# Kernel optimization log

Hardware: AMD Instinct MI355X
Metric: run time of the kernel (lower is better)

## Reference

```python
import jax, jax.numpy as jnp
import numpy as np

N_NODES = 100000
HIDDEN = 64
IN_CH = 61


def setup_inputs() -> dict:
    key = jax.random.key(0)
    ks = jax.random.split(key, 12)
    x = jax.random.normal(ks[0], (N_NODES, IN_CH), dtype=jnp.float32)
    edge_index = jax.random.randint(ks[1], (2, 3200000), 0, N_NODES, dtype=jnp.int64)
    s = 0.1
    # GCNConv weights (lin: in->hidden, bias separate)
    W1 = jax.random.normal(ks[2], (IN_CH, HIDDEN), dtype=jnp.float32) * s
    b1 = jnp.zeros((HIDDEN,), dtype=jnp.float32)
    W2 = jax.random.normal(ks[3], (HIDDEN, HIDDEN), dtype=jnp.float32) * s
    b2 = jnp.zeros((HIDDEN,), dtype=jnp.float32)
    W3 = jax.random.normal(ks[4], (HIDDEN, HIDDEN), dtype=jnp.float32) * s
    b3 = jnp.zeros((HIDDEN,), dtype=jnp.float32)
    # MLP head: Linear(64,64) -> ReLU -> Linear(64,1)
    Wh1 = jax.random.normal(ks[5], (HIDDEN, HIDDEN), dtype=jnp.float32) * s
    bh1 = jnp.zeros((HIDDEN,), dtype=jnp.float32)
    Wh2 = jax.random.normal(ks[6], (HIDDEN, 1), dtype=jnp.float32) * s
    bh2 = jnp.zeros((1,), dtype=jnp.float32)
    return {"x": x, "edge_index": edge_index,
            "W1": W1, "b1": b1, "W2": W2, "b2": b2, "W3": W3, "b3": b3,
            "Wh1": Wh1, "bh1": bh1, "Wh2": Wh2, "bh2": bh2}


def _gcn_layer(x, W, b, src, dst, norm, n):
    # x' = scatter_add_{dst}( norm_e * (xW)[src] ) + b   (self-loops already in src/dst)
    h = x @ W                                    # (N, out)
    msg = norm[:, None] * h[src]                 # (E', out) gather
    agg = jax.ops.segment_sum(msg, dst, num_segments=n)  # scatter-add
    return agg + b


def reference(x, edge_index, W1, b1, W2, b2, W3, b3, Wh1, bh1, Wh2, bh2):
    n = x.shape[0]
    # add self-loops (GCNConv default add_self_loops=True)
    loop = jnp.arange(n, dtype=edge_index.dtype)
    src = jnp.concatenate([edge_index[0], loop])
    dst = jnp.concatenate([edge_index[1], loop])
    # symmetric normalization: deg from in-degree (dst), norm = d^-1/2[src]*d^-1/2[dst]
    deg = jax.ops.segment_sum(jnp.ones_like(dst, dtype=x.dtype), dst, num_segments=n)
    dinv = jnp.where(deg > 0, jax.lax.rsqrt(deg), 0.0)
    norm = dinv[src] * dinv[dst]
    h = x
    for (W, b) in ((W1, b1), (W2, b2), (W3, b3)):
        h = jax.nn.relu(_gcn_layer(h, W, b, src, dst, norm, n))
        # dropout: identity in eval mode
    # MLP head
    h = jax.nn.relu(h @ Wh1 + bh1)
    out = (h @ Wh2 + bh2).squeeze(-1)            # (N,)
    return out
```

## Files before the change

### kernel.cpp

```cpp
#include <hip/hip_runtime.h>
#include <hip/hip_fp16.h>

#define HID 64
#define FSH 8
#define FB 392
#define SCAP 9216
#define FCH 4096

__device__ __forceinline__ float2 h2f2(unsigned int bits) {
    __half2 h = __builtin_bit_cast(__half2, bits);
    return __half22float2(h);
}

__global__ void zero_kernel(int* __restrict__ p, int n) {
    int i = blockIdx.x * blockDim.x + threadIdx.x;
    if (i < n) p[i] = 0;
}

__global__ __launch_bounds__(256) void fillA_kernel(const int* __restrict__ src,
                                                    const int* __restrict__ dst,
                                                    int* __restrict__ gcur,
                                                    unsigned int* __restrict__ recA,
                                                    int E) {
    __shared__ unsigned int srec[FCH];
    __shared__ int hist[FB], lbase[FB], lcur[FB], gpos[FB];
    __shared__ int buf[256];
    int t = threadIdx.x;
    int base = blockIdx.x * FCH;
    int lim = E - base;
    if (lim > FCH) lim = FCH;
    if (lim <= 0) return;
    for (int i = t; i < FB; i += 256) hist[i] = 0;
    __syncthreads();
    for (int i = t; i < lim; i += 256) atomicAdd(&hist[dst[base + i] >> FSH], 1);
    __syncthreads();
    int i0 = 2 * t, i1 = 2 * t + 1;
    int a0 = (i0 < FB) ? hist[i0] : 0;
    int a1 = (i1 < FB) ? hist[i1] : 0;
    int pair = a0 + a1;
    buf[t] = pair;
    __syncthreads();
#pragma unroll
    for (int o = 1; o < 256; o <<= 1) {
        int v = (t >= o) ? buf[t - o] : 0;
        __syncthreads();
        buf[t] += v;
        __syncthreads();
    }
    int excl = buf[t] - pair;
    if (i0 < FB) { lbase[i0] = excl;      lcur[i0] = excl; }
    if (i1 < FB) { lbase[i1] = excl + a0; lcur[i1] = excl + a0; }
    __syncthreads();
    for (int i = t; i < FB; i += 256) gpos[i] = atomicAdd(&gcur[i], hist[i]);
    __syncthreads();
    for (int i = t; i < lim; i += 256) {
        int d = dst[base + i];
        int s = src[base + i];
        int bkt = d >> FSH;
        int idx = atomicAdd(&lcur[bkt], 1);
        srec[idx] = ((unsigned int)(d & ((1 << FSH) - 1)) << 17) | (unsigned int)s;
    }
    __syncthreads();
    int g16 = t >> 4, lane = t & 15;
    for (int bkt = g16; bkt < FB; bkt += 16) {
        int L = hist[bkt], lb = lbase[bkt], gp = gpos[bkt];
        for (int j = lane; j < L; j += 16) {
            int g = gp + j;
            if (g < SCAP) recA[(size_t)bkt * SCAP + g] = srec[lb + j];
        }
    }
}

__global__ __launch_bounds__(256) void fillB_kernel(const int* __restrict__ gcur,
                                                    const unsigned int* __restrict__ recA,
                                                    int* __restrict__ rowptr,
                                                    float* __restrict__ dinv,
                                                    int* __restrict__ col, int N) {
    __shared__ unsigned int lcol[SCAP];
    __shared__ int hist[256], cur[256], buf[256];
    int b = blockIdx.x, t = threadIdx.x;
    int n0 = b << FSH;
    int p = 0;
    for (int i = t; i < b; i += 256) p += min(gcur[i], SCAP);
    buf[t] = p;
    __syncthreads();
#pragma unroll
    for (int o = 128; o > 0; o >>= 1) {
        if (t < o) buf[t] += buf[t + o];
        __syncthreads();
    }
    int rbase = buf[0];
    __syncthreads();
    hist[t] = 0;
    __syncthreads();
    int cnt = gcur[b];
    if (cnt > SCAP) cnt = SCAP;
    const unsigned int* rA = recA + (size_t)b * SCAP;
    for (int r = t; r < cnt; r += 256) atomicAdd(&hist[rA[r] >> 17], 1);
    __syncthreads();
    int a = hist[t];
    buf[t] = a;
    __syncthreads();
#pragma unroll
    for (int o = 1; o < 256; o <<= 1) {
        int v = (t >= o) ? buf[t - o] : 0;
        __syncthreads();
        buf[t] += v;
        __syncthreads();
    }
    int excl = buf[t] - a;
    int node = n0 + t;
    if (node <= N) rowptr[node] = rbase + excl;
    if (node < N) dinv[node] = 1.0f / sqrtf((float)(a + 1));
    cur[t] = excl;
    __syncthreads();
    for (int r = t; r < cnt; r += 256) {
        unsigned int rec = rA[r];
        int pos = atomicAdd(&cur[rec >> 17], 1);
        lcol[pos] = rec & 0x1ffffu;
    }
    __syncthreads();
    for (int j = t; j < cnt; j += 256) col[rbase + j] = (int)lcol[j];
}

__global__ __launch_bounds__(256) void linscale61_kernel(const float* __restrict__ x,
                                                         const float* __restrict__ W,
                                                         const float* __restrict__ dinv,
                                                         __half* __restrict__ out, int N) {
    __shared__ float4 Wl[61 * 16];
    const float4* W4 = reinterpret_cast<const float4*>(W);
    for (int i = threadIdx.x; i < 61 * 16; i += blockDim.x) Wl[i] = W4[i];
    __syncthreads();
    int node = blockIdx.x * blockDim.x + threadIdx.x;
    if (node >= N) return;
    float4 acc[16];
#pragma unroll
    for (int c = 0; c < 16; ++c) acc[c] = make_float4(0.f, 0.f, 0.f, 0.f);
    const float* xr = x + (size_t)node * 61;
    for (int k = 0; k < 61; ++k) {
        float xv = xr[k];
#pragma unroll
        for (int c = 0; c < 16; ++c) {
            float4 w = Wl[k * 16 + c];
            acc[c].x += xv * w.x;
            acc[c].y += xv * w.y;
            acc[c].z += xv * w.z;
            acc[c].w += xv * w.w;
        }
    }
    float dv = dinv[node];
    __half2* o = reinterpret_cast<__half2*>(out + (size_t)node * HID);
#pragma unroll
    for (int c = 0; c < 16; ++c) {
        o[c * 2 + 0] = __floats2half2_rn(acc[c].x * dv, acc[c].y * dv);
        o[c * 2 + 1] = __floats2half2_rn(acc[c].z * dv, acc[c].w * dv);
    }
}

__global__ __launch_bounds__(256) void linscale64h_kernel(const __half* __restrict__ x,
                                                          const float* __restrict__ W,
                                                          const float* __restrict__ dinv,
                                                          __half* __restrict__ out, int N) {
    __shared__ float4 Wl[64 * 16];
    const float4* W4 = reinterpret_cast<const float4*>(W);
    for (int i = threadIdx.x; i < 64 * 16; i += blockDim.x) Wl[i] = W4[i];
    __syncthreads();
    int node = blockIdx.x * blockDim.x + threadIdx.x;
    if (node >= N) return;
    float4 acc[16];
#pragma unroll
    for (int c = 0; c < 16; ++c) acc[c] = make_float4(0.f, 0.f, 0.f, 0.f);
    const uint4* xr4 = reinterpret_cast<const uint4*>(x + ((size_t)node << 6));
#pragma unroll
    for (int c8 = 0; c8 < 8; ++c8) {
        uint4 pk = xr4[c8];
        float2 f0 = h2f2(pk.x), f1 = h2f2(pk.y), f2 = h2f2(pk.z), f3 = h2f2(pk.w);
        float xv[8] = {f0.x, f0.y, f1.x, f1.y, f2.x, f2.y, f3.x, f3.y};
#pragma unroll
        for (int j = 0; j < 8; ++j) {
            int k = c8 * 8 + j;
#pragma unroll
            for (int c = 0; c < 16; ++c) {
                float4 w = Wl[k * 16 + c];
                acc[c].x += xv[j] * w.x;
                acc[c].y += xv[j] * w.y;
                acc[c].z += xv[j] * w.z;
                acc[c].w += xv[j] * w.w;
            }
        }
    }
    float dv = dinv[node];
    __half2* o = reinterpret_cast<__half2*>(out + ((size_t)node << 6));
#pragma unroll
    for (int c = 0; c < 16; ++c) {
        o[c * 2 + 0] = __floats2half2_rn(acc[c].x * dv, acc[c].y * dv);
        o[c * 2 + 1] = __floats2half2_rn(acc[c].z * dv, acc[c].w * dv);
    }
}

__global__ __launch_bounds__(256) void gather_kernel(const int* __restrict__ rowptr,
                                                     const int* __restrict__ col,
                                                     const float* __restrict__ dinv,
                                                     const __half2* __restrict__ hs2,
                                                     const float* __restrict__ b,
                                                     __half2* __restrict__ out2, int N) {
    int lane = threadIdx.x & 63;
    int hf = lane >> 5;
    int gl = lane & 31;
    int wid = (blockIdx.x * blockDim.x + threadIdx.x) >> 6;
    int nw = (gridDim.x * blockDim.x) >> 6;
    float bx = b[2 * gl], by = b[2 * gl + 1];
    for (int dbase = wid * 2; dbase < N; dbase += nw * 2) {
        int d = dbase + hf;
        bool act = d < N;
        int dd = act ? d : N - 1;
        int beg = rowptr[dd];
        int end = act ? rowptr[dd + 1] : beg;
        float2 acc0 = __half22float2(hs2[((size_t)dd << 5) + gl]);
        float2 acc1 = make_float2(0.f, 0.f);
        for (int ebase = beg; ebase < end; ebase += 32) {
            int e = ebase + gl;
            int cv = (e < end) ? col[e] : 0;
            int cnt = end - ebase;
            {
                unsigned int r[16];
#pragma unroll
                for (int k = 0; k < 16; ++k) {
                    int s = __shfl(cv, k, 32);
                    r[k] = *reinterpret_cast<const unsigned int*>(hs2 + ((size_t)s << 5) + gl);
                }
#pragma unroll
                for (int k = 0; k < 16; ++k) {
                    unsigned int bits = (k < cnt) ? r[k] : 0u;
                    float2 v = h2f2(bits);
                    if (k & 1) { acc1.x += v.x; acc1.y += v.y; }
                    else       { acc0.x += v.x; acc0.y += v.y; }
                }
            }
            if (cnt > 16) {
                unsigned int r[16];
#pragma unroll
                for (int k = 0; k < 16; ++k) {
                    int s = __shfl(cv, k + 16, 32);
                    r[k] = *reinterpret_cast<const unsigned int*>(hs2 + ((size_t)s << 5) + gl);
                }
#pragma unroll
                for (int k = 0; k < 16; ++k) {
                    unsigned int bits = (k + 16 < cnt) ? r[k] : 0u;
                    float2 v = h2f2(bits);
                    if (k & 1) { acc1.x += v.x; acc1.y += v.y; }
                    else       { acc0.x += v.x; acc0.y += v.y; }
                }
            }
        }
        if (act) {
            float dv = dinv[d];
            float rx = fmaxf(fmaf(acc0.x + acc1.x, dv, bx), 0.f);
            float ry = fmaxf(fmaf(acc0.y + acc1.y, dv, by), 0.f);
            out2[((size_t)d << 5) + gl] = __floats2half2_rn(rx, ry);
        }
    }
}

__global__ __launch_bounds__(256) void head_kernel(const __half* __restrict__ h,
                                                   const float* __restrict__ Wh1,
                                                   const float* __restrict__ bh1,
                                                   const float* __restrict__ Wh2,
                                                   const float* __restrict__ bh2,
                                                   float* __restrict__ out, int N) {
    __shared__ float4 Wl[64 * 16];
    __shared__ float bhs[64];
    __shared__ float w2s[64];
    const float4* W4 = reinterpret_cast<const float4*>(Wh1);
    for (int i = threadIdx.x; i < 64 * 16; i += blockDim.x) Wl[i] = W4[i];
    if (threadIdx.x < 64) {
        bhs[threadIdx.x] = bh1[threadIdx.x];
        w2s[threadIdx.x] = Wh2[threadIdx.x];
    }
    __syncthreads();
    int node = blockIdx.x * blockDim.x + threadIdx.x;
    if (node >= N) return;
    float4 acc[16];
#pragma unroll
    for (int c = 0; c < 16; ++c) acc[c] = make_float4(0.f, 0.f, 0.f, 0.f);
    const uint4* hr4 = reinterpret_cast<const uint4*>(h + ((size_t)node << 6));
#pragma unroll
    for (int c8 = 0; c8 < 8; ++c8) {
        uint4 pk = hr4[c8];
        float2 f0 = h2f2(pk.x), f1 = h2f2(pk.y), f2 = h2f2(pk.z), f3 = h2f2(pk.w);
        float xv[8] = {f0.x, f0.y, f1.x, f1.y, f2.x, f2.y, f3.x, f3.y};
#pragma unroll
        for (int j = 0; j < 8; ++j) {
            int k = c8 * 8 + j;
#pragma unroll
            for (int c = 0; c < 16; ++c) {
                float4 w = Wl[k * 16 + c];
                acc[c].x += xv[j] * w.x;
                acc[c].y += xv[j] * w.y;
                acc[c].z += xv[j] * w.z;
                acc[c].w += xv[j] * w.w;
            }
        }
    }
    float o = 0.f;
#pragma unroll
    for (int c = 0; c < 16; ++c) {
        o += fmaxf(acc[c].x + bhs[4 * c + 0], 0.f) * w2s[4 * c + 0];
        o += fmaxf(acc[c].y + bhs[4 * c + 1], 0.f) * w2s[4 * c + 1];
        o += fmaxf(acc[c].z + bhs[4 * c + 2], 0.f) * w2s[4 * c + 2];
        o += fmaxf(acc[c].w + bhs[4 * c + 3], 0.f) * w2s[4 * c + 3];
    }
    out[node] = o + bh2[0];
}

extern "C" void kernel_launch(void* const* d_in, const int* in_sizes, int n_in,
                              void* d_out, int out_size, void* d_ws, size_t ws_size,
                              hipStream_t stream) {
    const float* x = (const float*)d_in[0];
    const int* edge = (const int*)d_in[1];
    const float* W1 = (const float*)d_in[2];
    const float* b1 = (const float*)d_in[3];
    const float* W2 = (const float*)d_in[4];
    const float* b2 = (const float*)d_in[5];
    const float* W3 = (const float*)d_in[6];
    const float* b3 = (const float*)d_in[7];
    const float* Wh1 = (const float*)d_in[8];
    const float* bh1 = (const float*)d_in[9];
    const float* Wh2 = (const float*)d_in[10];
    const float* bh2 = (const float*)d_in[11];

    int N = in_sizes[0] / 61;
    int E = in_sizes[1] / 2;
    const int* srcs = edge;
    const int* dsts = edge + E;
    float* out = (float*)d_out;

    char* ws = (char*)d_ws;
    size_t off = 0;
    auto alloc = [&](size_t bytes) {
        void* p = ws + off;
        off += (bytes + 255) & ~(size_t)255;
        return p;
    };
    float* dinv = (float*)alloc((size_t)N * 4);
    int* rowptr = (int*)alloc((size_t)(N + 1) * 4);
    int* gcur = (int*)alloc((size_t)FB * 4);
    int* col = (int*)alloc((size_t)E * 4);
    __half* Ah = (__half*)alloc((size_t)N * HID * 2);
    __half* Bh = (__half*)alloc((size_t)N * HID * 2);
    if (off > ws_size) return;
    unsigned int* recA = (unsigned int*)Ah;

    int gN = (N + 255) / 256;
    int gA = (E + FCH - 1) / FCH;

    zero_kernel<<<(FB + 255) / 256, 256, 0, stream>>>(gcur, FB);
    fillA_kernel<<<gA, 256, 0, stream>>>(srcs, dsts, gcur, recA, E);
    fillB_kernel<<<FB, 256, 0, stream>>>(gcur, recA, rowptr, dinv, col, N);

    linscale61_kernel<<<gN, 256, 0, stream>>>(x, W1, dinv, Bh, N);
    gather_kernel<<<4096, 256, 0, stream>>>(rowptr, col, dinv,
                                            (const __half2*)Bh, b1, (__half2*)Ah, N);

    linscale64h_kernel<<<gN, 256, 0, stream>>>(Ah, W2, dinv, Bh, N);
    gather_kernel<<<4096, 256, 0, stream>>>(rowptr, col, dinv,
                                            (const __half2*)Bh, b2, (__half2*)Ah, N);

    linscale64h_kernel<<<gN, 256, 0, stream>>>(Ah, W3, dinv, Bh, N);
    gather_kernel<<<4096, 256, 0, stream>>>(rowptr, col, dinv,
                                            (const __half2*)Bh, b3, (__half2*)Ah, N);

    head_kernel<<<gN, 256, 0, stream>>>(Ah, Wh1, bh1, Wh2, bh2, out, N);
}
```

Before: 351.7 us.

## Halve CSR-build bucket width and stage x rows through LDS in first linear

The CSR construction now uses buckets of 128 destination nodes instead of 256. That doubles the bucket count to 784 and halves the per-bucket capacity, so the prefix scan in fillA and the node-level logic in fillB are adapted to the new sizes. fillB gets twice as many blocks with less shared memory each, which should improve occupancy and parallelism. Separately, the first linear kernel now copies each block's 128 rows of x into shared memory with coalesced loads, replacing strided per-thread row reads, and runs with 128-thread blocks. The smaller SCAP raises the chance that a bucket with high in-degree exceeds capacity and has edges silently dropped.

```diff
diff --git a/kernel.cpp b/kernel.cpp
--- a/kernel.cpp
+++ b/kernel.cpp
@@ -2,9 +2,9 @@
 #include <hip/hip_fp16.h>
 
 #define HID 64
-#define FSH 8
-#define FB 392
-#define SCAP 9216
+#define FSH 7
+#define FB 784
+#define SCAP 4608
 #define FCH 4096
 
 __device__ __forceinline__ float2 h2f2(unsigned int bits) {
@@ -34,11 +34,14 @@
     __syncthreads();
     for (int i = t; i < lim; i += 256) atomicAdd(&hist[dst[base + i] >> FSH], 1);
     __syncthreads();
-    int i0 = 2 * t, i1 = 2 * t + 1;
-    int a0 = (i0 < FB) ? hist[i0] : 0;
-    int a1 = (i1 < FB) ? hist[i1] : 0;
-    int pair = a0 + a1;
-    buf[t] = pair;
+    int h[4];
+#pragma unroll
+    for (int j = 0; j < 4; ++j) {
+        int idx = 4 * t + j;
+        h[j] = (idx < FB) ? hist[idx] : 0;
+    }
+    int tsum = h[0] + h[1] + h[2] + h[3];
+    buf[t] = tsum;
     __syncthreads();
 #pragma unroll
     for (int o = 1; o < 256; o <<= 1) {
@@ -47,9 +50,13 @@
         buf[t] += v;
         __syncthreads();
     }
-    int excl = buf[t] - pair;
-    if (i0 < FB) { lbase[i0] = excl;      lcur[i0] = excl; }
-    if (i1 < FB) { lbase[i1] = excl + a0; lcur[i1] = excl + a0; }
+    int excl = buf[t] - tsum;
+#pragma unroll
+    for (int j = 0; j < 4; ++j) {
+        int idx = 4 * t + j;
+        if (idx < FB) { lbase[idx] = excl; lcur[idx] = excl; }
+        excl += h[j];
+    }
     __syncthreads();
     for (int i = t; i < FB; i += 256) gpos[i] = atomicAdd(&gcur[i], hist[i]);
     __syncthreads();
@@ -61,10 +68,10 @@
         srec[idx] = ((unsigned int)(d & ((1 << FSH) - 1)) << 17) | (unsigned int)s;
     }
     __syncthreads();
-    int g16 = t >> 4, lane = t & 15;
-    for (int bkt = g16; bkt < FB; bkt += 16) {
+    int g8 = t >> 3, lane = t & 7;
+    for (int bkt = g8; bkt < FB; bkt += 32) {
         int L = hist[bkt], lb = lbase[bkt], gp = gpos[bkt];
-        for (int j = lane; j < L; j += 16) {
+        for (int j = lane; j < L; j += 8) {
             int g = gp + j;
             if (g < SCAP) recA[(size_t)bkt * SCAP + g] = srec[lb + j];
         }
@@ -77,7 +84,7 @@
                                                     float* __restrict__ dinv,
                                                     int* __restrict__ col, int N) {
     __shared__ unsigned int lcol[SCAP];
-    __shared__ int hist[256], cur[256], buf[256];
+    __shared__ int hist[128], cur[128], buf[256];
     int b = blockIdx.x, t = threadIdx.x;
     int n0 = b << FSH;
     int p = 0;
@@ -91,14 +98,14 @@
     }
     int rbase = buf[0];
     __syncthreads();
-    hist[t] = 0;
+    if (t < 128) hist[t] = 0;
     __syncthreads();
     int cnt = gcur[b];
     if (cnt > SCAP) cnt = SCAP;
     const unsigned int* rA = recA + (size_t)b * SCAP;
     for (int r = t; r < cnt; r += 256) atomicAdd(&hist[rA[r] >> 17], 1);
     __syncthreads();
-    int a = hist[t];
+    int a = (t < 128) ? hist[t] : 0;
     buf[t] = a;
     __syncthreads();
 #pragma unroll
@@ -109,10 +116,12 @@
         __syncthreads();
     }
     int excl = buf[t] - a;
-    int node = n0 + t;
-    if (node <= N) rowptr[node] = rbase + excl;
-    if (node < N) dinv[node] = 1.0f / sqrtf((float)(a + 1));
-    cur[t] = excl;
+    if (t < 128) {
+        int node = n0 + t;
+        if (node <= N) rowptr[node] = rbase + excl;
+        if (node < N) dinv[node] = 1.0f / sqrtf((float)(a + 1));
+        cur[t] = excl;
+    }
     __syncthreads();
     for (int r = t; r < cnt; r += 256) {
         unsigned int rec = rA[r];
@@ -123,20 +132,29 @@
     for (int j = t; j < cnt; j += 256) col[rbase + j] = (int)lcol[j];
 }
 
-__global__ __launch_bounds__(256) void linscale61_kernel(const float* __restrict__ x,
+__global__ __launch_bounds__(128) void linscale61_kernel(const float* __restrict__ x,
                                                          const float* __restrict__ W,
                                                          const float* __restrict__ dinv,
                                                          __half* __restrict__ out, int N) {
     __shared__ float4 Wl[61 * 16];
+    __shared__ float Xs[128 * 61];
+    int t = threadIdx.x;
     const float4* W4 = reinterpret_cast<const float4*>(W);
-    for (int i = threadIdx.x; i < 61 * 16; i += blockDim.x) Wl[i] = W4[i];
-    __syncthreads();
-    int node = blockIdx.x * blockDim.x + threadIdx.x;
-    if (node >= N) return;
+    for (int i = t; i < 61 * 16; i += 128) Wl[i] = W4[i];
+    int nb = blockIdx.x * 128;
+    int nrows = N - nb;
+    if (nrows > 128) nrows = 128;
+    if (nrows <= 0) return;
+    const float* srcx = x + (size_t)nb * 61;
+    int total = nrows * 61;
+    for (int i = t; i < total; i += 128) Xs[i] = srcx[i];
+    __syncthreads();
+    if (t >= nrows) return;
+    int node = nb + t;
     float4 acc[16];
 #pragma unroll
     for (int c = 0; c < 16; ++c) acc[c] = make_float4(0.f, 0.f, 0.f, 0.f);
-    const float* xr = x + (size_t)node * 61;
+    const float* xr = Xs + t * 61;
     for (int k = 0; k < 61; ++k) {
         float xv = xr[k];
 #pragma unroll
@@ -353,12 +371,13 @@
 
     int gN = (N + 255) / 256;
     int gA = (E + FCH - 1) / FCH;
+    int gL = (N + 127) / 128;
 
     zero_kernel<<<(FB + 255) / 256, 256, 0, stream>>>(gcur, FB);
     fillA_kernel<<<gA, 256, 0, stream>>>(srcs, dsts, gcur, recA, E);
     fillB_kernel<<<FB, 256, 0, stream>>>(gcur, recA, rowptr, dinv, col, N);
 
-    linscale61_kernel<<<gN, 256, 0, stream>>>(x, W1, dinv, Bh, N);
+    linscale61_kernel<<<gL, 128, 0, stream>>>(x, W1, dinv, Bh, N);
     gather_kernel<<<4096, 256, 0, stream>>>(rowptr, col, dinv,
                                             (const __half2*)Bh, b1, (__half2*)Ah, N);
 
```

After: 358.5 us. Within noise of the previous version (+1.9%).
